# Performance work log

Measured on AMD Instinct MI355X. Metric: run time of the kernel, lower is better.

The kernel has to match this reference:

```python
import jax, jax.numpy as jnp
import numpy as np

LEAKY = 0.1

def _leaky(x):
    return jax.nn.leaky_relu(x, LEAKY)

def _gather(pts, idx):
    # pts: [B, M, C], idx: [B, N, K] -> [B, N, K, C]
    return jax.vmap(lambda p, i: p[i])(pts, idx)

def _cross(xyz1, xyz2, p1, p2, pos_w, pos_b, mlps, k):
    # xyz1:[B,N1,3] xyz2:[B,N2,3] p1:[B,N1,D] p2:[B,N2,D]
    d = (jnp.sum(xyz1 * xyz1, -1)[:, :, None]
         + jnp.sum(xyz2 * xyz2, -1)[:, None, :]
         - 2.0 * jnp.einsum('bnc,bmc->bnm', xyz1, xyz2))  # [B,N1,N2]
    _, idx = jax.lax.top_k(-d, k)                          # smallest-k -> [B,N1,K]
    nb_xyz = _gather(xyz2, idx)                            # [B,N1,K,3]
    direction = nb_xyz - xyz1[:, :, None, :]
    g2 = _gather(p2, idx)                                  # [B,N1,K,D]
    posf = direction @ pos_w.T + pos_b                     # 1x1 conv on 3->D
    x = _leaky(g2 + p1[:, :, None, :] + posf)              # bn = Identity
    for w, b in mlps:
        x = _leaky(x @ w.T + b)                            # 1x1 Conv2d + bias + leaky
    return jnp.max(x, axis=2)                              # max-pool over K -> [B,N1,Cout]

def setup_inputs() -> dict:
    key = jax.random.key(0)
    ks = jax.random.split(key, 24)
    B, N, C, M1, M2, K = 2, 8192, 64, 64, 64, 16
    s = 0.1
    inp = {
        'pc1': jax.random.normal(ks[0], (B, 3, N), jnp.float32),
        'pc2': jax.random.normal(ks[1], (B, 3, N), jnp.float32),
        'feat1': jax.random.normal(ks[2], (B, C, N), jnp.float32),
        'feat2': jax.random.normal(ks[3], (B, C, N), jnp.float32),
        't11_w': jax.random.normal(ks[4], (M1, C), jnp.float32) * s,
        't11_b': jax.random.normal(ks[5], (M1,), jnp.float32) * s,
        't22_w': jax.random.normal(ks[6], (M1, C), jnp.float32) * s,
        't22_b': jax.random.normal(ks[7], (M1,), jnp.float32) * s,
        'pos1_w': jax.random.normal(ks[8], (M1, 3), jnp.float32) * s,
        'pos1_b': jax.random.normal(ks[9], (M1,), jnp.float32) * s,
        'mlp1_w1': jax.random.normal(ks[10], (M1, M1), jnp.float32) * s,
        'mlp1_b1': jax.random.normal(ks[11], (M1,), jnp.float32) * s,
        'mlp1_w2': jax.random.normal(ks[12], (M1, M1), jnp.float32) * s,
        'mlp1_b2': jax.random.normal(ks[13], (M1,), jnp.float32) * s,
        't1_w': jax.random.normal(ks[14], (M2, M1), jnp.float32) * s,
        't1_b': jax.random.normal(ks[15], (M2,), jnp.float32) * s,
        't2_w': jax.random.normal(ks[16], (M2, M1), jnp.float32) * s,
        't2_b': jax.random.normal(ks[17], (M2,), jnp.float32) * s,
        'pos2_w': jax.random.normal(ks[18], (M2, 3), jnp.float32) * s,
        'pos2_b': jax.random.normal(ks[19], (M2,), jnp.float32) * s,
        'mlp2_w1': jax.random.normal(ks[20], (M2, M2), jnp.float32) * s,
        'mlp2_b1': jax.random.normal(ks[21], (M2,), jnp.float32) * s,
    }
    return inp

def reference(pc1, pc2, feat1, feat2,
              t11_w, t11_b, t22_w, t22_b,
              pos1_w, pos1_b, mlp1_w1, mlp1_b1, mlp1_w2, mlp1_b2,
              t1_w, t1_b, t2_w, t2_b,
              pos2_w, pos2_b, mlp2_w1, mlp2_b1):
    K = 16
    x1 = jnp.transpose(pc1, (0, 2, 1))    # [B,N,3]
    x2 = jnp.transpose(pc2, (0, 2, 1))
    f1 = jnp.transpose(feat1, (0, 2, 1))  # [B,N,C]
    f2 = jnp.transpose(feat2, (0, 2, 1))
    mlp1 = [(mlp1_w1, mlp1_b1), (mlp1_w2, mlp1_b2)]
    mlp2 = [(mlp2_w1, mlp2_b1)]
    # feat1_new = cross_t1(cross(pc1, pc2, t11(feat1), t22(feat2), pos1, mlp1))
    q1 = f1 @ t11_w.T + t11_b
    q2 = f2 @ t22_w.T + t22_b
    fn1 = _cross(x1, x2, q1, q2, pos1_w, pos1_b, mlp1, K) @ t1_w.T + t1_b  # [B,N,M2]
    # feat2_new = cross_t2(cross(pc2, pc1, t11(feat2), t22(feat1), pos1, mlp1))
    r1 = f2 @ t11_w.T + t11_b
    r2 = f1 @ t22_w.T + t22_b
    fn2 = _cross(x2, x1, r1, r2, pos1_w, pos1_b, mlp1, K) @ t2_w.T + t2_b  # [B,N,M2]
    # feat1_final = cross(pc1, pc2, feat1_new, feat2_new, pos2, mlp2)
    ff = _cross(x1, x2, fn1, fn2, pos2_w, pos2_b, mlp2, K)                 # [B,N,M2]
    to_cn = lambda a: jnp.transpose(a, (0, 2, 1))  # back to [B,C,N] torch layout
    return (to_cn(fn1), to_cn(fn2), to_cn(ff))
```

## Files before the change

kernel.cpp:

```cpp
#include <hip/hip_runtime.h>

#define NPTS 8192
#define BATCH 2
#define CC 64
#define KNN 16

typedef __attribute__((ext_vector_type(4))) float  f32x4;
typedef __attribute__((ext_vector_type(8))) short  s16x8;

__device__ __forceinline__ unsigned short f2bf(float f) {
  unsigned u = __float_as_uint(f);
  unsigned r = ((u >> 16) & 1u) + 0x7FFFu;
  return (unsigned short)((u + r) >> 16);
}

__device__ __forceinline__ float leaky(float v) { return fmaxf(v, 0.1f * v); }

__device__ __forceinline__ s16x8 pack8(const float v[8]) {
  union { s16x8 v8; unsigned short s[8]; } u;
  #pragma unroll
  for (int j = 0; j < 8; ++j) u.s[j] = f2bf(v[j]);
  return u.v8;
}

__global__ __launch_bounds__(256) void kprep(const float* __restrict__ pc1,
                                             const float* __restrict__ pc2,
                                             float4* __restrict__ x1t,
                                             float4* __restrict__ x2t) {
  int i = blockIdx.x * 256 + threadIdx.x;
  int b = i >> 13, n = i & (NPTS - 1);
  size_t base = (size_t)b * 3 * NPTS + n;
  float x = pc1[base], y = pc1[base + NPTS], z = pc1[base + 2 * NPTS];
  x1t[i] = make_float4(x, y, z, x * x + y * y + z * z);
  x = pc2[base]; y = pc2[base + NPTS]; z = pc2[base + 2 * NPTS];
  x2t[i] = make_float4(x, y, z, x * x + y * y + z * z);
}

__global__ __launch_bounds__(256) void ktrans(
    const float* __restrict__ f1, const float* __restrict__ f2,
    const float* __restrict__ w11, const float* __restrict__ b11,
    const float* __restrict__ w22, const float* __restrict__ b22,
    float* __restrict__ q1, float* __restrict__ q2,
    float* __restrict__ r1, float* __restrict__ r2) {
  const int z = blockIdx.z;
  const float* in = (z == 0 || z == 3) ? f1 : f2;
  const float* W  = (z == 0 || z == 2) ? w11 : w22;
  const float* Bb = (z == 0 || z == 2) ? b11 : b22;
  float* out = (z == 0) ? q1 : (z == 1) ? q2 : (z == 2) ? r1 : r2;
  const int b = blockIdx.y;
  const int n0 = blockIdx.x * 64;
  const int t = threadIdx.x;

  __shared__ float ft[64 * 65];
  __shared__ float wt[64 * 68];

  #pragma unroll
  for (int j = 0; j < 16; ++j) {
    int e = t + 256 * j;
    int c = e >> 6, tn = e & 63;
    ft[c * 65 + tn] = in[((size_t)b * 64 + c) * NPTS + n0 + tn];
  }
  #pragma unroll
  for (int j = 0; j < 16; ++j) {
    int e = t + 256 * j;
    int mm = e >> 6, c = e & 63;
    wt[c * 68 + mm] = W[e];
  }
  __syncthreads();

  const int tn = t & 63, mg = t >> 6;
  float a[16];
  #pragma unroll
  for (int u = 0; u < 4; ++u) {
    float4 bb = *(const float4*)&Bb[16 * mg + 4 * u];
    a[4 * u] = bb.x; a[4 * u + 1] = bb.y; a[4 * u + 2] = bb.z; a[4 * u + 3] = bb.w;
  }
  for (int c = 0; c < 64; ++c) {
    float x = ft[c * 65 + tn];
    #pragma unroll
    for (int u = 0; u < 4; ++u) {
      float4 w4 = *(const float4*)&wt[c * 68 + 16 * mg + 4 * u];
      a[4 * u]     = fmaf(x, w4.x, a[4 * u]);
      a[4 * u + 1] = fmaf(x, w4.y, a[4 * u + 1]);
      a[4 * u + 2] = fmaf(x, w4.z, a[4 * u + 2]);
      a[4 * u + 3] = fmaf(x, w4.w, a[4 * u + 3]);
    }
  }
  size_t ob = ((size_t)b * NPTS + n0 + tn) * 64 + 16 * mg;
  #pragma unroll
  for (int u = 0; u < 4; ++u)
    *(float4*)&out[ob + 4 * u] =
        make_float4(a[4 * u], a[4 * u + 1], a[4 * u + 2], a[4 * u + 3]);
}

__device__ __forceinline__ void kinsert(unsigned key, unsigned ii,
                                        unsigned (&D)[16], unsigned (&I)[16]) {
  if (key < D[15]) {
    bool lt[16];
    #pragma unroll
    for (int j = 0; j < 16; ++j) lt[j] = key < D[j];
    #pragma unroll
    for (int j = 15; j >= 1; --j) {
      D[j] = lt[j - 1] ? D[j - 1] : (lt[j] ? key : D[j]);
      I[j] = lt[j - 1] ? I[j - 1] : (lt[j] ? ii  : I[j]);
    }
    if (lt[0]) { D[0] = key; I[0] = ii; }
  }
}

#define CHUNKS 8
#define CHSZ (NPTS / CHUNKS)
#define RDEPTH 28
#define RTRIG 20

__global__ __launch_bounds__(256) void kknn(const float4* __restrict__ x1t,
                                            const float4* __restrict__ x2t,
                                            uint2* __restrict__ part) {
  const int dir = blockIdx.z;
  const int b = blockIdx.y;
  const float4* xq = dir ? x2t : x1t;
  const float4* xc = dir ? x1t : x2t;
  const int t = threadIdx.x;
  const int qb = blockIdx.x & 31;
  const int ck = blockIdx.x >> 5;
  const int qi = qb * 256 + t;

  __shared__ float4 tile[CHSZ];
  __shared__ unsigned short ring[RDEPTH][256];

  const float4* src = xc + (size_t)b * NPTS + ck * CHSZ;
  #pragma unroll
  for (int j = 0; j < CHSZ / 256; ++j) tile[j * 256 + t] = src[j * 256 + t];

  float4 Q = xq[(size_t)b * NPTS + qi];
  const float nqx = -2.f * Q.x, nqy = -2.f * Q.y, nqz = -2.f * Q.z, qn = Q.w;

  unsigned D[16], I[16];
  #pragma unroll
  for (int j = 0; j < 16; ++j) { D[j] = 0xFFFFFFFFu; I[j] = 0u; }
  int cnt = 0;

  __syncthreads();

  const unsigned ibase = (unsigned)(ck * CHSZ);
  for (int j0 = 0; j0 < CHSZ; j0 += 8) {
    unsigned D15 = D[15];
    #pragma unroll
    for (int u = 0; u < 8; ++u) {
      float4 C = tile[j0 + u];
      float d = fmaf(C.x, nqx, fmaf(C.y, nqy, fmaf(C.z, nqz, qn + C.w)));
      unsigned key = (unsigned)max((int)__float_as_uint(d), 0);
      ring[cnt][t] = (unsigned short)(j0 + u);
      cnt += (key < D15) ? 1 : 0;
    }
    if (__any(cnt >= RTRIG)) {
      for (int e = 0; e < cnt; ++e) {
        int ji = ring[e][t];
        float4 C = tile[ji];
        float d = fmaf(C.x, nqx, fmaf(C.y, nqy, fmaf(C.z, nqz, qn + C.w)));
        unsigned key = (unsigned)max((int)__float_as_uint(d), 0);
        kinsert(key, ibase + ji, D, I);
      }
      cnt = 0;
    }
  }
  for (int e = 0; e < cnt; ++e) {
    int ji = ring[e][t];
    float4 C = tile[ji];
    float d = fmaf(C.x, nqx, fmaf(C.y, nqy, fmaf(C.z, nqz, qn + C.w)));
    unsigned key = (unsigned)max((int)__float_as_uint(d), 0);
    kinsert(key, ibase + ji, D, I);
  }

  uint2* pb = part + ((size_t)(((dir << 1) | b) * CHUNKS + ck) * 16) * NPTS;
  #pragma unroll
  for (int j = 0; j < 16; ++j)
    pb[(size_t)j * NPTS + qi] = make_uint2(D[j], I[j]);
}

__global__ __launch_bounds__(256) void kmerge(const uint2* __restrict__ part,
                                              int* __restrict__ idx12,
                                              int* __restrict__ idx21) {
  const int dir = blockIdx.z, b = blockIdx.y;
  const int qi = blockIdx.x * 256 + threadIdx.x;
  const uint2* pb = part + ((size_t)(((dir << 1) | b) * CHUNKS) * 16) * NPTS;

  unsigned D[16], I[16];
  #pragma unroll
  for (int j = 0; j < 16; ++j) {
    uint2 kv = pb[(size_t)j * NPTS + qi];
    D[j] = kv.x; I[j] = kv.y;
  }
  for (int ck = 1; ck < CHUNKS; ++ck) {
    #pragma unroll
    for (int j = 0; j < 16; ++j) {
      uint2 kv = pb[(size_t)(ck * 16 + j) * NPTS + qi];
      kinsert(kv.x, kv.y, D, I);
    }
  }
  int* out = dir ? idx21 : idx12;
  size_t ob = ((size_t)b * NPTS + qi) * 16;
  #pragma unroll
  for (int j = 0; j < 16; ++j) out[ob + j] = (int)I[j];
}

template <int NL>
__global__ __launch_bounds__(256) void kcross(
    const float4* __restrict__ xq0, const float4* __restrict__ xc0, const int* __restrict__ idx0,
    const float* __restrict__ p10, const float* __restrict__ p20,
    float* __restrict__ orm0, float* __restrict__ ocn0,
    const float4* __restrict__ xq1, const float4* __restrict__ xc1, const int* __restrict__ idx1,
    const float* __restrict__ p11, const float* __restrict__ p21,
    float* __restrict__ orm1, float* __restrict__ ocn1,
    const float* __restrict__ posw, const float* __restrict__ posb,
    const float* __restrict__ w1, const float* __restrict__ b1,
    const float* __restrict__ w2, const float* __restrict__ b2) {
  const float4* xq; const float4* xc; const int* idx; const float* p1; const float* p2;
  float* orm; float* ocn;
  if (blockIdx.y == 0) { xq = xq0; xc = xc0; idx = idx0; p1 = p10; p2 = p20; orm = orm0; ocn = ocn0; }
  else                 { xq = xq1; xc = xc1; idx = idx1; p1 = p11; p2 = p21; orm = orm1; ocn = ocn1; }

  __shared__ float4 pw4[64];
  __shared__ __align__(16) unsigned short ylds[4][16 * 72];

  const int t = threadIdx.x;
  const int lane = t & 63;
  const int w = t >> 6;
  const int m = lane & 15;
  const int q = lane >> 4;

  if (t < 64) pw4[t] = make_float4(posw[t * 3], posw[t * 3 + 1], posw[t * 3 + 2], posb[t]);
  __syncthreads();

  s16x8 wf[2][4][2];
  float bv[2][4];
  #pragma unroll
  for (int l = 0; l < NL; ++l) {
    const float* Wl = l ? w2 : w1;
    const float* Bl = l ? b2 : b1;
    #pragma unroll
    for (int ct = 0; ct < 4; ++ct) {
      bv[l][ct] = Bl[16 * ct + m];
      const float* rowp = Wl + (size_t)(16 * ct + m) * 64;
      #pragma unroll
      for (int kt = 0; kt < 2; ++kt) {
        const float* pp = rowp + 32 * kt + 8 * q;
        float4 A  = *(const float4*)pp;
        float4 Bq = *(const float4*)(pp + 4);
        float vv[8] = {A.x, A.y, A.z, A.w, Bq.x, Bq.y, Bq.z, Bq.w};
        wf[l][ct][kt] = pack8(vv);
      }
    }
  }

  unsigned short* yw = &ylds[w][0];
  const f32x4 zz = {0.f, 0.f, 0.f, 0.f};

  #pragma unroll 1
  for (int i = 0; i < 4; ++i) {
    int gp = blockIdx.x * 16 + w * 4 + i;
    int b = gp >> 13, n = gp & (NPTS - 1);
    size_t qb = (size_t)b * NPTS + n;
    int nb = idx[qb * 16 + m];
    size_t cb = (size_t)b * NPTS + nb;
    float4 qp  = xq[qb];
    float4 nbp = xc[cb];
    float dx = nbp.x - qp.x, dy = nbp.y - qp.y, dz = nbp.z - qp.z;

    s16x8 af[2];
    #pragma unroll
    for (int h = 0; h < 2; ++h) {
      int c0 = 32 * h + 8 * q;
      const float* g2p = p2 + cb * 64 + c0;
      float4 ga = *(const float4*)g2p;
      float4 gb = *(const float4*)(g2p + 4);
      const float* p1p = p1 + qb * 64 + c0;
      float4 pa = *(const float4*)p1p;
      float4 pb = *(const float4*)(p1p + 4);
      float gg[8] = {ga.x + pa.x, ga.y + pa.y, ga.z + pa.z, ga.w + pa.w,
                     gb.x + pb.x, gb.y + pb.y, gb.z + pb.z, gb.w + pb.w};
      float vv[8];
      #pragma unroll
      for (int j = 0; j < 8; ++j) {
        float4 pw = pw4[c0 + j];
        float v = gg[j] + pw.w;
        v = fmaf(dx, pw.x, v);
        v = fmaf(dy, pw.y, v);
        v = fmaf(dz, pw.z, v);
        vv[j] = leaky(v);
      }
      af[h] = pack8(vv);
    }

    f32x4 acc[4];
    #pragma unroll
    for (int ct = 0; ct < 4; ++ct) {
      acc[ct] = __builtin_amdgcn_mfma_f32_16x16x32_bf16(af[0], wf[0][ct][0], zz, 0, 0, 0);
      acc[ct] = __builtin_amdgcn_mfma_f32_16x16x32_bf16(af[1], wf[0][ct][1], acc[ct], 0, 0, 0);
    }
    float y[4][4];
    #pragma unroll
    for (int ct = 0; ct < 4; ++ct)
      #pragma unroll
      for (int r = 0; r < 4; ++r)
        y[ct][r] = leaky(acc[ct][r] + bv[0][ct]);

    if (NL == 2) {
      #pragma unroll
      for (int ct = 0; ct < 4; ++ct)
        #pragma unroll
        for (int r = 0; r < 4; ++r)
          yw[(q * 4 + r) * 72 + 16 * ct + m] = f2bf(y[ct][r]);
      asm volatile("s_waitcnt lgkmcnt(0)" ::: "memory");
      s16x8 a2[2];
      a2[0] = *(const s16x8*)(yw + m * 72 + 8 * q);
      a2[1] = *(const s16x8*)(yw + m * 72 + 32 + 8 * q);
      #pragma unroll
      for (int ct = 0; ct < 4; ++ct) {
        acc[ct] = __builtin_amdgcn_mfma_f32_16x16x32_bf16(a2[0], wf[1][ct][0], zz, 0, 0, 0);
        acc[ct] = __builtin_amdgcn_mfma_f32_16x16x32_bf16(a2[1], wf[1][ct][1], acc[ct], 0, 0, 0);
      }
      #pragma unroll
      for (int ct = 0; ct < 4; ++ct)
        #pragma unroll
        for (int r = 0; r < 4; ++r)
          y[ct][r] = leaky(acc[ct][r] + bv[1][ct]);
      asm volatile("s_waitcnt lgkmcnt(0)" ::: "memory");
    }

    float pm[4];
    #pragma unroll
    for (int ct = 0; ct < 4; ++ct) {
      float v = fmaxf(fmaxf(y[ct][0], y[ct][1]), fmaxf(y[ct][2], y[ct][3]));
      v = fmaxf(v, __shfl_xor(v, 16));
      v = fmaxf(v, __shfl_xor(v, 32));
      pm[ct] = v;
    }
    float sel = (q == 0) ? pm[0] : (q == 1) ? pm[1] : (q == 2) ? pm[2] : pm[3];
    if (orm) orm[qb * 64 + lane] = sel;
    if (ocn) ocn[((size_t)b * 64 + lane) * NPTS + n] = sel;
  }
}

__global__ __launch_bounds__(256) void kpost(
    const float* __restrict__ inA, const float* __restrict__ inB,
    const float* __restrict__ wA, const float* __restrict__ bA,
    const float* __restrict__ wB, const float* __restrict__ bB,
    float* __restrict__ frA, float* __restrict__ frB,
    float* __restrict__ cnA, float* __restrict__ cnB) {
  const int z = blockIdx.z;
  const float* in = z ? inB : inA;
  const float* W  = z ? wB : wA;
  const float* Bb = z ? bB : bA;
  float* fr = z ? frB : frA;
  float* cn = z ? cnB : cnA;
  const int b = blockIdx.y;
  const int n0 = blockIdx.x * 64;
  const int t = threadIdx.x;

  __shared__ float pl[64 * 65];
  __shared__ float wt[64 * 68];

  #pragma unroll
  for (int j = 0; j < 16; ++j) {
    int e = t + 256 * j;
    int r = e >> 6, c = e & 63;
    pl[r * 65 + c] = in[((size_t)b * NPTS + n0 + r) * 64 + c];
  }
  #pragma unroll
  for (int j = 0; j < 16; ++j) {
    int e = t + 256 * j;
    int mm = e >> 6, c = e & 63;
    wt[c * 68 + mm] = W[e];
  }
  __syncthreads();

  const int tn = t & 63, mg = t >> 6;
  float a[16];
  #pragma unroll
  for (int u = 0; u < 4; ++u) {
    float4 bb = *(const float4*)&Bb[16 * mg + 4 * u];
    a[4 * u] = bb.x; a[4 * u + 1] = bb.y; a[4 * u + 2] = bb.z; a[4 * u + 3] = bb.w;
  }
  for (int c = 0; c < 64; ++c) {
    float x = pl[tn * 65 + c];
    #pragma unroll
    for (int u = 0; u < 4; ++u) {
      float4 w4 = *(const float4*)&wt[c * 68 + 16 * mg + 4 * u];
      a[4 * u]     = fmaf(x, w4.x, a[4 * u]);
      a[4 * u + 1] = fmaf(x, w4.y, a[4 * u + 1]);
      a[4 * u + 2] = fmaf(x, w4.z, a[4 * u + 2]);
      a[4 * u + 3] = fmaf(x, w4.w, a[4 * u + 3]);
    }
  }
  size_t ob = ((size_t)b * NPTS + n0 + tn) * 64 + 16 * mg;
  #pragma unroll
  for (int u = 0; u < 4; ++u)
    *(float4*)&fr[ob + 4 * u] =
        make_float4(a[4 * u], a[4 * u + 1], a[4 * u + 2], a[4 * u + 3]);
  #pragma unroll
  for (int jj = 0; jj < 16; ++jj) {
    int mo = 16 * mg + jj;
    cn[((size_t)b * 64 + mo) * NPTS + n0 + tn] = a[jj];
  }
}

extern "C" void kernel_launch(void* const* d_in, const int* in_sizes, int n_in,
                              void* d_out, int out_size, void* d_ws, size_t ws_size,
                              hipStream_t stream) {
  const float* pc1   = (const float*)d_in[0];
  const float* pc2   = (const float*)d_in[1];
  const float* feat1 = (const float*)d_in[2];
  const float* feat2 = (const float*)d_in[3];
  const float* t11w  = (const float*)d_in[4];
  const float* t11b  = (const float*)d_in[5];
  const float* t22w  = (const float*)d_in[6];
  const float* t22b  = (const float*)d_in[7];
  const float* pos1w = (const float*)d_in[8];
  const float* pos1b = (const float*)d_in[9];
  const float* m1w1  = (const float*)d_in[10];
  const float* m1b1  = (const float*)d_in[11];
  const float* m1w2  = (const float*)d_in[12];
  const float* m1b2  = (const float*)d_in[13];
  const float* t1w   = (const float*)d_in[14];
  const float* t1b   = (const float*)d_in[15];
  const float* t2w   = (const float*)d_in[16];
  const float* t2b   = (const float*)d_in[17];
  const float* pos2w = (const float*)d_in[18];
  const float* pos2b = (const float*)d_in[19];
  const float* m2w1  = (const float*)d_in[20];
  const float* m2b1  = (const float*)d_in[21];

  char* ws = (char*)d_ws;
  size_t off = 0;
  auto take = [&](size_t bytes) {
    char* p = ws + off;
    off += (bytes + 255) & ~(size_t)255;
    return p;
  };
  float4* x1t  = (float4*)take((size_t)BATCH * NPTS * sizeof(float4));
  float4* x2t  = (float4*)take((size_t)BATCH * NPTS * sizeof(float4));
  int* idx12   = (int*)take((size_t)BATCH * NPTS * KNN * 4);
  int* idx21   = (int*)take((size_t)BATCH * NPTS * KNN * 4);
  float* q1    = (float*)take((size_t)BATCH * NPTS * CC * 4);
  float* q2    = (float*)take((size_t)BATCH * NPTS * CC * 4);
  float* r1    = (float*)take((size_t)BATCH * NPTS * CC * 4);
  float* r2    = (float*)take((size_t)BATCH * NPTS * CC * 4);
  float* poolA = (float*)take((size_t)BATCH * NPTS * CC * 4);
  float* poolB = (float*)take((size_t)BATCH * NPTS * CC * 4);
  float* fn1   = (float*)take((size_t)BATCH * NPTS * CC * 4);
  float* fn2   = (float*)take((size_t)BATCH * NPTS * CC * 4);
  take((size_t)2 * 1024 * 1024);
  uint2* part  = (uint2*)q1;

  float* out = (float*)d_out;
  size_t seg = (size_t)BATCH * CC * NPTS;

  kprep<<<dim3(BATCH * NPTS / 256), 256, 0, stream>>>(pc1, pc2, x1t, x2t);
  kknn<<<dim3(32 * CHUNKS, BATCH, 2), 256, 0, stream>>>(x1t, x2t, part);
  kmerge<<<dim3(NPTS / 256, BATCH, 2), 256, 0, stream>>>(part, idx12, idx21);
  ktrans<<<dim3(NPTS / 64, BATCH, 4), 256, 0, stream>>>(
      feat1, feat2, t11w, t11b, t22w, t22b, q1, q2, r1, r2);
  kcross<2><<<dim3(1024, 2), 256, 0, stream>>>(
      x1t, x2t, idx12, q1, q2, poolA, (float*)nullptr,
      x2t, x1t, idx21, r1, r2, poolB, (float*)nullptr,
      pos1w, pos1b, m1w1, m1b1, m1w2, m1b2);
  kpost<<<dim3(NPTS / 64, BATCH, 2), 256, 0, stream>>>(
      poolA, poolB, t1w, t1b, t2w, t2b, fn1, fn2, out, out + seg);
  kcross<1><<<dim3(1024, 1), 256, 0, stream>>>(
      x1t, x2t, idx12, fn1, fn2, (float*)nullptr, out + 2 * seg,
      x1t, x2t, idx12, fn1, fn2, (float*)nullptr, (float*)nullptr,
      pos2w, pos2b, m2w1, m2b1, m2w1, m2b1);
}
```

Measured before the change: 462.6 us.

## Screen KNN candidates with bf16 split-precision MFMA distance tiles

```diff
diff --git a/kernel.cpp b/kernel.cpp
--- a/kernel.cpp
+++ b/kernel.cpp
@@ -7,33 +7,73 @@
 
 typedef __attribute__((ext_vector_type(4))) float  f32x4;
 typedef __attribute__((ext_vector_type(8))) short  s16x8;
-
-__device__ __forceinline__ unsigned short f2bf(float f) {
+typedef unsigned short u16;
+
+__device__ __forceinline__ u16 f2bf(float f) {
   unsigned u = __float_as_uint(f);
   unsigned r = ((u >> 16) & 1u) + 0x7FFFu;
-  return (unsigned short)((u + r) >> 16);
+  return (u16)((u + r) >> 16);
 }
 
 __device__ __forceinline__ float leaky(float v) { return fmaxf(v, 0.1f * v); }
 
 __device__ __forceinline__ s16x8 pack8(const float v[8]) {
-  union { s16x8 v8; unsigned short s[8]; } u;
+  union { s16x8 v8; u16 s[8]; } u;
   #pragma unroll
   for (int j = 0; j < 8; ++j) u.s[j] = f2bf(v[j]);
   return u.v8;
+}
+
+__device__ __forceinline__ void split2(float v, u16& h, u16& l) {
+  h = f2bf(v);
+  float hf = __uint_as_float((unsigned)h << 16);
+  l = f2bf(v - hf);
 }
 
 __global__ __launch_bounds__(256) void kprep(const float* __restrict__ pc1,
                                              const float* __restrict__ pc2,
                                              float4* __restrict__ x1t,
-                                             float4* __restrict__ x2t) {
+                                             float4* __restrict__ x2t,
+                                             u16* __restrict__ arow1, u16* __restrict__ arow2,
+                                             u16* __restrict__ brow1, u16* __restrict__ brow2) {
   int i = blockIdx.x * 256 + threadIdx.x;
   int b = i >> 13, n = i & (NPTS - 1);
   size_t base = (size_t)b * 3 * NPTS + n;
-  float x = pc1[base], y = pc1[base + NPTS], z = pc1[base + 2 * NPTS];
-  x1t[i] = make_float4(x, y, z, x * x + y * y + z * z);
-  x = pc2[base]; y = pc2[base + NPTS]; z = pc2[base + 2 * NPTS];
-  x2t[i] = make_float4(x, y, z, x * x + y * y + z * z);
+  #pragma unroll
+  for (int c = 0; c < 2; ++c) {
+    const float* pc = c ? pc2 : pc1;
+    float4* xt = c ? x2t : x1t;
+    u16* ar = c ? arow2 : arow1;
+    u16* br = c ? brow2 : brow1;
+    float x = pc[base], y = pc[base + NPTS], z = pc[base + 2 * NPTS];
+    float w = x * x + y * y + z * z;
+    xt[i] = make_float4(x, y, z, w);
+    u16 A[32];
+    #pragma unroll
+    for (int j = 0; j < 32; ++j) A[j] = 0;
+    u16 h, l;
+    split2(-2.f * x, h, l); A[0] = h; A[1] = l; A[2] = h;
+    split2(-2.f * y, h, l); A[3] = h; A[4] = l; A[5] = h;
+    split2(-2.f * z, h, l); A[6] = h; A[7] = l; A[8] = h;
+    split2(w, h, l);        A[9] = h; A[10] = l;
+    A[11] = 0x3F80; A[12] = 0x3F80;
+    uint4* ap = (uint4*)(ar + (size_t)i * 32);
+    ap[0] = ((const uint4*)A)[0];
+    ap[1] = ((const uint4*)A)[1];
+    ap[2] = ((const uint4*)A)[2];
+    ap[3] = ((const uint4*)A)[3];
+    u16 Bv[16];
+    #pragma unroll
+    for (int j = 0; j < 16; ++j) Bv[j] = 0;
+    split2(x, h, l); Bv[0] = h; Bv[1] = h; Bv[2] = l;
+    split2(y, h, l); Bv[3] = h; Bv[4] = h; Bv[5] = l;
+    split2(z, h, l); Bv[6] = h; Bv[7] = h; Bv[8] = l;
+    Bv[9] = 0x3F80; Bv[10] = 0x3F80;
+    split2(w, h, l); Bv[11] = h; Bv[12] = l;
+    uint4* bp = (uint4*)(br + (size_t)i * 16);
+    bp[0] = ((const uint4*)Bv)[0];
+    bp[1] = ((const uint4*)Bv)[1];
+  }
 }
 
 __global__ __launch_bounds__(256) void ktrans(
@@ -108,74 +148,147 @@
   }
 }
 
-#define CHUNKS 8
-#define CHSZ (NPTS / CHUNKS)
-#define RDEPTH 28
-#define RTRIG 20
-
-__global__ __launch_bounds__(256) void kknn(const float4* __restrict__ x1t,
-                                            const float4* __restrict__ x2t,
-                                            uint2* __restrict__ part) {
+__device__ __forceinline__ void klex(unsigned key, unsigned ii,
+                                     unsigned (&D)[16], unsigned (&I)[16]) {
+  if ((key < D[15]) || (key == D[15] && ii < I[15])) {
+    bool lt[16];
+    #pragma unroll
+    for (int j = 0; j < 16; ++j) lt[j] = (key < D[j]) || (key == D[j] && ii < I[j]);
+    #pragma unroll
+    for (int j = 15; j >= 1; --j) {
+      D[j] = lt[j - 1] ? D[j - 1] : (lt[j] ? key : D[j]);
+      I[j] = lt[j - 1] ? I[j - 1] : (lt[j] ? ii  : I[j]);
+    }
+    if (lt[0]) { D[0] = key; I[0] = ii; }
+  }
+}
+
+#define CH 4
+#define CKSZ (NPTS / CH)
+#define RD 15
+#define RT 11
+#define FDELTA 0.008f
+#define KINF 0x7F7FFFFFu
+
+__global__ __launch_bounds__(256) void kknn(
+    const float4* __restrict__ x1t, const float4* __restrict__ x2t,
+    const u16* __restrict__ arow1, const u16* __restrict__ arow2,
+    const u16* __restrict__ brow1, const u16* __restrict__ brow2,
+    uint2* __restrict__ part) {
   const int dir = blockIdx.z;
   const int b = blockIdx.y;
   const float4* xq = dir ? x2t : x1t;
   const float4* xc = dir ? x1t : x2t;
+  const u16* ar = dir ? arow1 : arow2;
+  const u16* br = dir ? brow2 : brow1;
   const int t = threadIdx.x;
-  const int qb = blockIdx.x & 31;
-  const int ck = blockIdx.x >> 5;
-  const int qi = qb * 256 + t;
-
-  __shared__ float4 tile[CHSZ];
-  __shared__ unsigned short ring[RDEPTH][256];
-
-  const float4* src = xc + (size_t)b * NPTS + ck * CHSZ;
-  #pragma unroll
-  for (int j = 0; j < CHSZ / 256; ++j) tile[j * 256 + t] = src[j * 256 + t];
-
-  float4 Q = xq[(size_t)b * NPTS + qi];
+  const int lane = t & 63;
+  const int w = t >> 6;
+  const int m = lane & 15;
+  const int kh = lane >> 4;
+  const int qb = blockIdx.x & 127;
+  const int ck = blockIdx.x >> 7;
+
+  __shared__ float4 cxyz[CKSZ];
+  __shared__ u16 ring[RD][256];
+
+  const size_t cb = (size_t)b * NPTS + ck * CKSZ;
+  #pragma unroll
+  for (int j = 0; j < CKSZ / 256; ++j) cxyz[j * 256 + t] = xc[cb + j * 256 + t];
+
+  const int qi = qb * 64 + w * 16 + m;
+  const size_t qg = (size_t)b * NPTS + qi;
+  float4 Q = xq[qg];
   const float nqx = -2.f * Q.x, nqy = -2.f * Q.y, nqz = -2.f * Q.z, qn = Q.w;
 
+  s16x8 bf;
+  if (kh < 2) bf = *(const s16x8*)(br + qg * 16 + kh * 8);
+  else { s16x8 zb = {0,0,0,0,0,0,0,0}; bf = zb; }
+
   unsigned D[16], I[16];
   #pragma unroll
-  for (int j = 0; j < 16; ++j) { D[j] = 0xFFFFFFFFu; I[j] = 0u; }
+  for (int j = 0; j < 16; ++j) { D[j] = KINF; I[j] = 0u; }
+  float tf = __uint_as_float(KINF);
   int cnt = 0;
 
   __syncthreads();
 
-  const unsigned ibase = (unsigned)(ck * CHSZ);
-  for (int j0 = 0; j0 < CHSZ; j0 += 8) {
-    unsigned D15 = D[15];
-    #pragma unroll
-    for (int u = 0; u < 8; ++u) {
-      float4 C = tile[j0 + u];
-      float d = fmaf(C.x, nqx, fmaf(C.y, nqy, fmaf(C.z, nqz, qn + C.w)));
-      unsigned key = (unsigned)max((int)__float_as_uint(d), 0);
-      ring[cnt][t] = (unsigned short)(j0 + u);
-      cnt += (key < D15) ? 1 : 0;
-    }
-    if (__any(cnt >= RTRIG)) {
+  const unsigned ibase = (unsigned)(ck * CKSZ);
+  const u16* arb = ar + cb * 32;
+  const f32x4 zz = {0.f, 0.f, 0.f, 0.f};
+
+  s16x8 afC = *(const s16x8*)(arb + (size_t)m * 32 + kh * 8);
+
+  for (int step = 0; step < CKSZ / 16; ++step) {
+    s16x8 afN = *(const s16x8*)(arb + (size_t)((step + 1) * 16 + m) * 32 + kh * 8);
+    f32x4 acc = __builtin_amdgcn_mfma_f32_16x16x32_bf16(afC, bf, zz, 0, 0, 0);
+    int crow = step * 16 + kh * 4;
+    #pragma unroll
+    for (int r = 0; r < 4; ++r) {
+      ring[cnt][t] = (u16)(crow + r);
+      cnt += (acc[r] < tf) ? 1 : 0;
+    }
+    if (__any(cnt >= RT)) {
       for (int e = 0; e < cnt; ++e) {
         int ji = ring[e][t];
-        float4 C = tile[ji];
+        float4 C = cxyz[ji];
         float d = fmaf(C.x, nqx, fmaf(C.y, nqy, fmaf(C.z, nqz, qn + C.w)));
         unsigned key = (unsigned)max((int)__float_as_uint(d), 0);
         kinsert(key, ibase + ji, D, I);
       }
       cnt = 0;
-    }
+      unsigned s15 = min(D[15], (unsigned)__shfl_xor((int)D[15], 16));
+      s15 = min(s15, (unsigned)__shfl_xor((int)s15, 32));
+      s15 = min(s15, KINF);
+      tf = __uint_as_float(s15) + FDELTA;
+    }
+    afC = afN;
   }
   for (int e = 0; e < cnt; ++e) {
     int ji = ring[e][t];
-    float4 C = tile[ji];
+    float4 C = cxyz[ji];
     float d = fmaf(C.x, nqx, fmaf(C.y, nqy, fmaf(C.z, nqz, qn + C.w)));
     unsigned key = (unsigned)max((int)__float_as_uint(d), 0);
     kinsert(key, ibase + ji, D, I);
   }
 
-  uint2* pb = part + ((size_t)(((dir << 1) | b) * CHUNKS + ck) * 16) * NPTS;
-  #pragma unroll
-  for (int j = 0; j < 16; ++j)
-    pb[(size_t)j * NPTS + qi] = make_uint2(D[j], I[j]);
+  unsigned LD[16], LI[16];
+  #pragma unroll
+  for (int j = 0; j < 16; ++j) {
+    unsigned od = (unsigned)__shfl_xor((int)D[15 - j], 16);
+    unsigned oi = (unsigned)__shfl_xor((int)I[15 - j], 16);
+    bool take = (D[j] < od) || (D[j] == od && I[j] < oi);
+    LD[j] = take ? D[j] : od;
+    LI[j] = take ? I[j] : oi;
+  }
+  #pragma unroll
+  for (int dd = 8; dd >= 1; dd >>= 1) {
+    #pragma unroll
+    for (int j = 0; j < 16; ++j) {
+      if (!(j & dd)) {
+        int k2 = j + dd;
+        bool sw = (LD[j] > LD[k2]) || (LD[j] == LD[k2] && LI[j] > LI[k2]);
+        unsigned tk = LD[j], ti = LI[j];
+        LD[j] = sw ? LD[k2] : LD[j];  LI[j] = sw ? LI[k2] : LI[j];
+        LD[k2] = sw ? tk : LD[k2];    LI[k2] = sw ? ti : LI[k2];
+      }
+    }
+  }
+  unsigned MD[16], MI[16];
+  #pragma unroll
+  for (int j = 0; j < 16; ++j) {
+    unsigned od = (unsigned)__shfl_xor((int)LD[15 - j], 32);
+    unsigned oi = (unsigned)__shfl_xor((int)LI[15 - j], 32);
+    bool take = (LD[j] < od) || (LD[j] == od && LI[j] < oi);
+    MD[j] = take ? LD[j] : od;
+    MI[j] = take ? LI[j] : oi;
+  }
+  if (kh == 0) {
+    uint2* pb = part + ((size_t)((dir * 2 + b) * CH + ck) * 16) * NPTS;
+    #pragma unroll
+    for (int j = 0; j < 16; ++j)
+      pb[(size_t)j * NPTS + qi] = make_uint2(MD[j], MI[j]);
+  }
 }
 
 __global__ __launch_bounds__(256) void kmerge(const uint2* __restrict__ part,
@@ -183,19 +296,16 @@
                                               int* __restrict__ idx21) {
   const int dir = blockIdx.z, b = blockIdx.y;
   const int qi = blockIdx.x * 256 + threadIdx.x;
-  const uint2* pb = part + ((size_t)(((dir << 1) | b) * CHUNKS) * 16) * NPTS;
+  const uint2* pb = part + ((size_t)((dir * 2 + b) * CH) * 16) * NPTS;
 
   unsigned D[16], I[16];
   #pragma unroll
-  for (int j = 0; j < 16; ++j) {
-    uint2 kv = pb[(size_t)j * NPTS + qi];
-    D[j] = kv.x; I[j] = kv.y;
-  }
-  for (int ck = 1; ck < CHUNKS; ++ck) {
+  for (int j = 0; j < 16; ++j) { D[j] = KINF; I[j] = 0u; }
+  for (int l = 0; l < CH; ++l) {
     #pragma unroll
     for (int j = 0; j < 16; ++j) {
-      uint2 kv = pb[(size_t)(ck * 16 + j) * NPTS + qi];
-      kinsert(kv.x, kv.y, D, I);
+      uint2 kv = pb[(size_t)(l * 16 + j) * NPTS + qi];
+      klex(kv.x, kv.y, D, I);
     }
   }
   int* out = dir ? idx21 : idx12;
@@ -221,7 +331,7 @@
   else                 { xq = xq1; xc = xc1; idx = idx1; p1 = p11; p2 = p21; orm = orm1; ocn = ocn1; }
 
   __shared__ float4 pw4[64];
-  __shared__ __align__(16) unsigned short ylds[4][16 * 72];
+  __shared__ __align__(16) u16 ylds[4][16 * 72];
 
   const int t = threadIdx.x;
   const int lane = t & 63;
@@ -253,7 +363,7 @@
     }
   }
 
-  unsigned short* yw = &ylds[w][0];
+  u16* yw = &ylds[w][0];
   const f32x4 zz = {0.f, 0.f, 0.f, 0.f};
 
   #pragma unroll 1
@@ -442,6 +552,10 @@
   float4* x2t  = (float4*)take((size_t)BATCH * NPTS * sizeof(float4));
   int* idx12   = (int*)take((size_t)BATCH * NPTS * KNN * 4);
   int* idx21   = (int*)take((size_t)BATCH * NPTS * KNN * 4);
+  u16* arow1   = (u16*)take(((size_t)BATCH * NPTS + 16) * 64);
+  u16* arow2   = (u16*)take(((size_t)BATCH * NPTS + 16) * 64);
+  u16* brow1   = (u16*)take((size_t)BATCH * NPTS * 32);
+  u16* brow2   = (u16*)take((size_t)BATCH * NPTS * 32);
   float* q1    = (float*)take((size_t)BATCH * NPTS * CC * 4);
   float* q2    = (float*)take((size_t)BATCH * NPTS * CC * 4);
   float* r1    = (float*)take((size_t)BATCH * NPTS * CC * 4);
@@ -450,14 +564,15 @@
   float* poolB = (float*)take((size_t)BATCH * NPTS * CC * 4);
   float* fn1   = (float*)take((size_t)BATCH * NPTS * CC * 4);
   float* fn2   = (float*)take((size_t)BATCH * NPTS * CC * 4);
-  take((size_t)2 * 1024 * 1024);
-  uint2* part  = (uint2*)q1;
+  uint2* part  = (uint2*)take((size_t)4 * CH * 16 * NPTS * sizeof(uint2));
 
   float* out = (float*)d_out;
   size_t seg = (size_t)BATCH * CC * NPTS;
 
-  kprep<<<dim3(BATCH * NPTS / 256), 256, 0, stream>>>(pc1, pc2, x1t, x2t);
-  kknn<<<dim3(32 * CHUNKS, BATCH, 2), 256, 0, stream>>>(x1t, x2t, part);
+  kprep<<<dim3(BATCH * NPTS / 256), 256, 0, stream>>>(
+      pc1, pc2, x1t, x2t, arow1, arow2, brow1, brow2);
+  kknn<<<dim3(128 * CH, BATCH, 2), 256, 0, stream>>>(
+      x1t, x2t, arow1, arow2, brow1, brow2, part);
   kmerge<<<dim3(NPTS / 256, BATCH, 2), 256, 0, stream>>>(part, idx12, idx21);
   ktrans<<<dim3(NPTS / 64, BATCH, 4), 256, 0, stream>>>(
       feat1, feat2, t11w, t11b, t22w, t22b, q1, q2, r1, r2);
```

Measured after the change: 517.7 us. +11.9%, slower.

## Split KNN into cold chunks and threshold-seeded warm chunks

Applied to the files above, without the earlier changes.

```diff
diff --git a/kernel.cpp b/kernel.cpp
--- a/kernel.cpp
+++ b/kernel.cpp
@@ -7,17 +7,18 @@
 
 typedef __attribute__((ext_vector_type(4))) float  f32x4;
 typedef __attribute__((ext_vector_type(8))) short  s16x8;
-
-__device__ __forceinline__ unsigned short f2bf(float f) {
+typedef unsigned short u16;
+
+__device__ __forceinline__ u16 f2bf(float f) {
   unsigned u = __float_as_uint(f);
   unsigned r = ((u >> 16) & 1u) + 0x7FFFu;
-  return (unsigned short)((u + r) >> 16);
+  return (u16)((u + r) >> 16);
 }
 
 __device__ __forceinline__ float leaky(float v) { return fmaxf(v, 0.1f * v); }
 
 __device__ __forceinline__ s16x8 pack8(const float v[8]) {
-  union { s16x8 v8; unsigned short s[8]; } u;
+  union { s16x8 v8; u16 s[8]; } u;
   #pragma unroll
   for (int j = 0; j < 8; ++j) u.s[j] = f2bf(v[j]);
   return u.v8;
@@ -110,12 +111,14 @@
 
 #define CHUNKS 8
 #define CHSZ (NPTS / CHUNKS)
-#define RDEPTH 28
-#define RTRIG 20
-
-__global__ __launch_bounds__(256) void kknn(const float4* __restrict__ x1t,
-                                            const float4* __restrict__ x2t,
-                                            uint2* __restrict__ part) {
+#define NCOLD 2
+
+#define ARD 20
+#define ART 12
+
+__global__ __launch_bounds__(256) void kknnA(const float4* __restrict__ x1t,
+                                             const float4* __restrict__ x2t,
+                                             uint2* __restrict__ part) {
   const int dir = blockIdx.z;
   const int b = blockIdx.y;
   const float4* xq = dir ? x2t : x1t;
@@ -126,7 +129,7 @@
   const int qi = qb * 256 + t;
 
   __shared__ float4 tile[CHSZ];
-  __shared__ unsigned short ring[RDEPTH][256];
+  __shared__ uint2 ring[ARD][256];
 
   const float4* src = xc + (size_t)b * NPTS + ck * CHSZ;
   #pragma unroll
@@ -138,22 +141,97 @@
   unsigned D[16], I[16];
   #pragma unroll
   for (int j = 0; j < 16; ++j) { D[j] = 0xFFFFFFFFu; I[j] = 0u; }
+
+  __syncthreads();
+
+  const unsigned ibase = (unsigned)(ck * CHSZ);
+  #pragma unroll
+  for (int j = 0; j < 16; ++j) {
+    float4 C = tile[j];
+    float d = fmaf(C.x, nqx, fmaf(C.y, nqy, fmaf(C.z, nqz, qn + C.w)));
+    unsigned key = (unsigned)max((int)__float_as_uint(d), 0);
+    kinsert(key, ibase + j, D, I);
+  }
+
   int cnt = 0;
-
-  __syncthreads();
-
-  const unsigned ibase = (unsigned)(ck * CHSZ);
-  for (int j0 = 0; j0 < CHSZ; j0 += 8) {
+  for (int j0 = 16; j0 < CHSZ; j0 += 8) {
     unsigned D15 = D[15];
     #pragma unroll
     for (int u = 0; u < 8; ++u) {
       float4 C = tile[j0 + u];
       float d = fmaf(C.x, nqx, fmaf(C.y, nqy, fmaf(C.z, nqz, qn + C.w)));
       unsigned key = (unsigned)max((int)__float_as_uint(d), 0);
-      ring[cnt][t] = (unsigned short)(j0 + u);
+      ring[cnt][t] = make_uint2(key, ibase + j0 + u);
       cnt += (key < D15) ? 1 : 0;
     }
-    if (__any(cnt >= RTRIG)) {
+    if (__any(cnt >= ART)) {
+      for (int e = 0; e < cnt; ++e) {
+        uint2 kv = ring[e][t];
+        kinsert(kv.x, kv.y, D, I);
+      }
+      cnt = 0;
+    }
+  }
+  for (int e = 0; e < cnt; ++e) {
+    uint2 kv = ring[e][t];
+    kinsert(kv.x, kv.y, D, I);
+  }
+
+  uint2* pb = part + ((size_t)(((dir << 1) | b) * CHUNKS + ck) * 16) * NPTS;
+  #pragma unroll
+  for (int j = 0; j < 16; ++j)
+    pb[(size_t)j * NPTS + qi] = make_uint2(D[j], I[j]);
+}
+
+#define BRD 24
+#define BRT 16
+
+__global__ __launch_bounds__(256) void kknnB(const float4* __restrict__ x1t,
+                                             const float4* __restrict__ x2t,
+                                             uint2* __restrict__ part) {
+  const int dir = blockIdx.z;
+  const int b = blockIdx.y;
+  const float4* xq = dir ? x2t : x1t;
+  const float4* xc = dir ? x1t : x2t;
+  const int t = threadIdx.x;
+  const int qb = blockIdx.x & 31;
+  const int ck = NCOLD + (blockIdx.x >> 5);
+  const int qi = qb * 256 + t;
+
+  __shared__ float4 tile[CHSZ];
+  __shared__ u16 ring[BRD][256];
+
+  const float4* src = xc + (size_t)b * NPTS + ck * CHSZ;
+  #pragma unroll
+  for (int j = 0; j < CHSZ / 256; ++j) tile[j * 256 + t] = src[j * 256 + t];
+
+  float4 Q = xq[(size_t)b * NPTS + qi];
+  const float nqx = -2.f * Q.x, nqy = -2.f * Q.y, nqz = -2.f * Q.z, qn = Q.w;
+
+  const size_t gb = (size_t)(((dir << 1) | b) * CHUNKS) * 16 * NPTS;
+  unsigned ta = part[gb + (size_t)15 * NPTS + qi].x;
+  unsigned tb = part[gb + (size_t)(16 + 15) * NPTS + qi].x;
+  const unsigned tfB = min(ta, tb) + 1u;
+
+  unsigned D[16], I[16];
+  #pragma unroll
+  for (int j = 0; j < 16; ++j) { D[j] = 0xFFFFFFFFu; I[j] = 0u; }
+  int cnt = 0;
+
+  __syncthreads();
+
+  const unsigned ibase = (unsigned)(ck * CHSZ);
+  for (int j0 = 0; j0 < CHSZ; j0 += 8) {
+    unsigned w = min(D[15], tfB);
+    #pragma unroll
+    for (int u = 0; u < 8; ++u) {
+      float4 C = tile[j0 + u];
+      float d = fmaf(C.x, nqx, fmaf(C.y, nqy, fmaf(C.z, nqz, qn + C.w)));
+      unsigned key = (unsigned)max((int)__float_as_uint(d), 0);
+      ring[cnt][t] = (u16)(j0 + u);
+      cnt += (key < w) ? 1 : 0;
+    }
+    if (__any(cnt >= BRT)) {
       for (int e = 0; e < cnt; ++e) {
         int ji = ring[e][t];
         float4 C = tile[ji];
@@ -221,7 +299,7 @@
   else                 { xq = xq1; xc = xc1; idx = idx1; p1 = p11; p2 = p21; orm = orm1; ocn = ocn1; }
 
   __shared__ float4 pw4[64];
-  __shared__ __align__(16) unsigned short ylds[4][16 * 72];
+  __shared__ __align__(16) u16 ylds[4][16 * 72];
 
   const int t = threadIdx.x;
   const int lane = t & 63;
@@ -253,7 +331,7 @@
     }
   }
 
-  unsigned short* yw = &ylds[w][0];
+  u16* yw = &ylds[w][0];
   const f32x4 zz = {0.f, 0.f, 0.f, 0.f};
 
   #pragma unroll 1
@@ -457,7 +535,8 @@
   size_t seg = (size_t)BATCH * CC * NPTS;
 
   kprep<<<dim3(BATCH * NPTS / 256), 256, 0, stream>>>(pc1, pc2, x1t, x2t);
-  kknn<<<dim3(32 * CHUNKS, BATCH, 2), 256, 0, stream>>>(x1t, x2t, part);
+  kknnA<<<dim3(32 * NCOLD, BATCH, 2), 256, 0, stream>>>(x1t, x2t, part);
+  kknnB<<<dim3(32 * (CHUNKS - NCOLD), BATCH, 2), 256, 0, stream>>>(x1t, x2t, part);
   kmerge<<<dim3(NPTS / 256, BATCH, 2), 256, 0, stream>>>(part, idx12, idx21);
   ktrans<<<dim3(NPTS / 64, BATCH, 4), 256, 0, stream>>>(
       feat1, feat2, t11w, t11b, t22w, t22b, q1, q2, r1, r2);
```

After: 463.6 us. Within noise of the previous version (+0.2%).
